# Kernel optimization log

Measured on AMD Instinct MI355X. Metric: run time of the kernel, lower is better.

## Reference

```python
import jax, jax.numpy as jnp
import numpy as np

DECAY_CONSTANT = 1.0


def _build_decay_matrices(weight, decay_value, S, dtype):
    """Build the row-repeat and col-repeat upper-triangular decay matrices.

    Wr[i, j] = w0[i] * (clip(dv0,0.9,1) ** (j-i) / C)   for j >= i, else 0
    Wc[i, j] = w1[j] *  clip(dv1,0.9,1) ** ((j-i) / C)  for j >= i, else 0
    """
    i = jnp.arange(S)[:, None]
    j = jnp.arange(S)[None, :]
    mask = j >= i
    # Clamp exponent to 0 in the masked-out (lower-triangular) region so the
    # power never overflows; values there are discarded by the mask anyway.
    e = jnp.where(mask, (j - i).astype(dtype), jnp.asarray(0.0, dtype))
    dv0 = jnp.clip(decay_value[0, 0], 0.9, 1.0).astype(dtype)
    dv1 = jnp.clip(decay_value[1, 0], 0.9, 1.0).astype(dtype)
    w0 = weight[0].astype(dtype)
    w1 = weight[1].astype(dtype)
    Wr = jnp.where(mask, w0[:, None] * ((dv0 ** e) / DECAY_CONSTANT), jnp.asarray(0.0, dtype))
    Wc = jnp.where(mask, w1[None, :] * (dv1 ** (e / DECAY_CONSTANT)), jnp.asarray(0.0, dtype))
    return Wr, Wc


def setup_inputs() -> dict:
    key = jax.random.key(0)
    kx, kw = jax.random.split(key)
    B, E, S = 4, 2048, 2048
    x = jax.random.normal(kx, (B, E, S), dtype=jnp.float32)
    weight = jax.random.normal(kw, (2, S), dtype=jnp.float32)
    bias = jnp.zeros((S,), dtype=jnp.float32)
    decay_value = jnp.ones((2, 1), dtype=jnp.float32)
    return {"x": x, "weight": weight, "bias": bias, "decay_value": decay_value}


def reference(x, weight, bias, decay_value):
    B, E, S = x.shape
    Wr, Wc = _build_decay_matrices(weight, decay_value, S, x.dtype)
    # x @ Wr + x @ Wc == x @ (Wr + Wc); contract the S axis.
    out = jnp.einsum('bes,st->bet', x, Wr + Wc)  # [B, E, S]
    out = out + bias.astype(x.dtype)
    return out
```

## Files before the change

### kernel.cpp

```cpp
#include <hip/hip_runtime.h>


#define S_LEN 2048
#define THREADS 256

__global__ __launch_bounds__(THREADS, 8)
void crcl_kernel(const float* __restrict__ x,
                 const float* __restrict__ weight,
                 const float* __restrict__ bias,
                 const float* __restrict__ decay,
                 float* __restrict__ out)
{
    __shared__ float carry[2][4];

    const int t    = (int)threadIdx.x;
    const int lane = t & 63;
    const int w    = t >> 6;
    const long row = (long)blockIdx.x;

    const float4* x4  = (const float4*)(x + row * (long)S_LEN);
    const float4* w04 = (const float4*)weight;
    const float4* w14 = (const float4*)(weight + S_LEN);
    const float4* b4  = (const float4*)bias;

    const float4 xa = x4[2 * t],  xb = x4[2 * t + 1];
    const float4 wa = w04[2 * t], wb = w04[2 * t + 1];
    const float4 va = w14[2 * t], vb = w14[2 * t + 1];
    const float4 ba = b4[2 * t],  bb = b4[2 * t + 1];

    const float dv0 = fminf(fmaxf(decay[0], 0.9f), 1.0f);
    const float dv1 = fminf(fmaxf(decay[1], 0.9f), 1.0f);

    const float xs[8] = {xa.x, xa.y, xa.z, xa.w, xb.x, xb.y, xb.z, xb.w};
    const float ws[8] = {wa.x, wa.y, wa.z, wa.w, wb.x, wb.y, wb.z, wb.w};

    float pc = 0.0f, qc = 0.0f;
#pragma unroll
    for (int k = 0; k < 8; ++k) {
        pc = fmaf(dv0, pc, xs[k] * ws[k]);
        qc = fmaf(dv1, qc, xs[k]);
    }

    float A8_0 = dv0 * dv0; A8_0 *= A8_0; A8_0 *= A8_0;
    float A8_1 = dv1 * dv1; A8_1 *= A8_1; A8_1 *= A8_1;

    float cp = pc, cq = qc;
    float k0 = A8_0, k1 = A8_1;
#pragma unroll
    for (int d = 1; d < 64; d <<= 1) {
        const float up = __shfl_up(cp, (unsigned)d, 64);
        const float uq = __shfl_up(cq, (unsigned)d, 64);
        if (lane >= d) {
            cp = fmaf(k0, up, cp);
            cq = fmaf(k1, uq, cq);
        }
        k0 *= k0;
        k1 *= k1;
    }
    float cin_p = __shfl_up(cp, 1u, 64);
    float cin_q = __shfl_up(cq, 1u, 64);
    if (lane == 0) { cin_p = 0.0f; cin_q = 0.0f; }

    if (lane == 63) { carry[0][w] = cp; carry[1][w] = cq; }
    __syncthreads();

    float A512_0 = A8_0, A512_1 = A8_1;
#pragma unroll
    for (int b = 0; b < 6; ++b) { A512_0 *= A512_0; A512_1 *= A512_1; }

    float cwp = 0.0f, cwq = 0.0f;
#pragma unroll
    for (int v = 0; v < 3; ++v) {
        if (v < w) {
            cwp = fmaf(cwp, A512_0, carry[0][v]);
            cwq = fmaf(cwq, A512_1, carry[1][v]);
        }
    }
    const float e8 = (float)(8 * lane);
    const float pwl_0 = exp2f(e8 * log2f(dv0));
    const float pwl_1 = exp2f(e8 * log2f(dv1));
    cin_p = fmaf(cwp, pwl_0, cin_p);
    cin_q = fmaf(cwq, pwl_1, cin_q);

    const float vs[8] = {va.x, va.y, va.z, va.w, vb.x, vb.y, vb.z, vb.w};
    const float bs[8] = {ba.x, ba.y, ba.z, ba.w, bb.x, bb.y, bb.z, bb.w};

    float p2 = cin_p, q2 = cin_q;
    float ys[8];
#pragma unroll
    for (int k = 0; k < 8; ++k) {
        p2 = fmaf(dv0, p2, xs[k] * ws[k]);
        q2 = fmaf(dv1, q2, xs[k]);
        ys[k] = fmaf(vs[k], q2, p2) + bs[k];
    }

    float4* o4 = (float4*)(out + row * (long)S_LEN);
    o4[2 * t]     = make_float4(ys[0], ys[1], ys[2], ys[3]);
    o4[2 * t + 1] = make_float4(ys[4], ys[5], ys[6], ys[7]);
}

extern "C" void kernel_launch(void* const* d_in, const int* in_sizes, int n_in,
                              void* d_out, int out_size, void* d_ws, size_t ws_size,
                              hipStream_t stream) {
    const float* x      = (const float*)d_in[0];
    const float* weight = (const float*)d_in[1];
    const float* bias   = (const float*)d_in[2];
    const float* decay  = (const float*)d_in[3];
    float* out = (float*)d_out;

    const int nrows = in_sizes[0] / S_LEN;
    hipLaunchKernelGGL(crcl_kernel, dim3(nrows), dim3(THREADS), 0, stream,
                       x, weight, bias, decay, out);
}
```

Measured before the change: 27.13 us.

## Split each row into two coalesced halves with interleaved scans

Each thread now loads float4s at index t and 256+t instead of two adjacent float4s, so every global load and store instruction touches a fully contiguous span across the wavefront. To keep the recurrence correct, two independent 4-element chunks are scanned per thread in parallel. The block-level carry combine is extended to eight wave segments. This doubles the wave-level shuffle scans in exchange for better-coalesced memory access and more independent work per step.

```diff
diff --git a/kernel.cpp b/kernel.cpp
--- a/kernel.cpp
+++ b/kernel.cpp
@@ -3,6 +3,8 @@
 
 #define S_LEN 2048
 #define THREADS 256
+
+typedef float f4 __attribute__((ext_vector_type(4)));
 
 __global__ __launch_bounds__(THREADS, 8)
 void crcl_kernel(const float* __restrict__ x,
@@ -11,92 +13,119 @@
                  const float* __restrict__ decay,
                  float* __restrict__ out)
 {
-    __shared__ float carry[2][4];
+    __shared__ float ctot[2][8];
 
     const int t    = (int)threadIdx.x;
     const int lane = t & 63;
     const int w    = t >> 6;
     const long row = (long)blockIdx.x;
 
-    const float4* x4  = (const float4*)(x + row * (long)S_LEN);
-    const float4* w04 = (const float4*)weight;
-    const float4* w14 = (const float4*)(weight + S_LEN);
-    const float4* b4  = (const float4*)bias;
+    const f4* x4  = (const f4*)(x + row * (long)S_LEN);
+    const f4* w04 = (const f4*)weight;
+    const f4* w14 = (const f4*)(weight + S_LEN);
+    const f4* b4  = (const f4*)bias;
 
-    const float4 xa = x4[2 * t],  xb = x4[2 * t + 1];
-    const float4 wa = w04[2 * t], wb = w04[2 * t + 1];
-    const float4 va = w14[2 * t], vb = w14[2 * t + 1];
-    const float4 ba = b4[2 * t],  bb = b4[2 * t + 1];
+    const int sA = t, sB = 256 + t;
+    const f4 xA = x4[sA],  xB = x4[sB];
+    const f4 wA = w04[sA], wB = w04[sB];
+    const f4 vA = w14[sA], vB = w14[sB];
+    const f4 bA = b4[sA],  bB = b4[sB];
 
     const float dv0 = fminf(fmaxf(decay[0], 0.9f), 1.0f);
     const float dv1 = fminf(fmaxf(decay[1], 0.9f), 1.0f);
 
-    const float xs[8] = {xa.x, xa.y, xa.z, xa.w, xb.x, xb.y, xb.z, xb.w};
-    const float ws[8] = {wa.x, wa.y, wa.z, wa.w, wb.x, wb.y, wb.z, wb.w};
+    float A4_0 = dv0 * dv0; A4_0 *= A4_0;
+    float A4_1 = dv1 * dv1; A4_1 *= A4_1;
+    float A256_0 = A4_0, A256_1 = A4_1;
+#pragma unroll
+    for (int b = 0; b < 6; ++b) { A256_0 *= A256_0; A256_1 *= A256_1; }
+    const float e4 = (float)(4 * lane);
+    const float pw0l = exp2f(e4 * log2f(dv0));
+    const float pw1l = exp2f(e4 * log2f(dv1));
 
-    float pc = 0.0f, qc = 0.0f;
+    float TAp = 0.0f, TAq = 0.0f, TBp = 0.0f, TBq = 0.0f;
 #pragma unroll
-    for (int k = 0; k < 8; ++k) {
-        pc = fmaf(dv0, pc, xs[k] * ws[k]);
-        qc = fmaf(dv1, qc, xs[k]);
+    for (int j = 0; j < 4; ++j) {
+        TAp = fmaf(dv0, TAp, xA[j] * wA[j]);
+        TAq = fmaf(dv1, TAq, xA[j]);
+        TBp = fmaf(dv0, TBp, xB[j] * wB[j]);
+        TBq = fmaf(dv1, TBq, xB[j]);
     }
 
-    float A8_0 = dv0 * dv0; A8_0 *= A8_0; A8_0 *= A8_0;
-    float A8_1 = dv1 * dv1; A8_1 *= A8_1; A8_1 *= A8_1;
-
-    float cp = pc, cq = qc;
-    float k0 = A8_0, k1 = A8_1;
+    float sAp = TAp, sAq = TAq, sBp = TBp, sBq = TBq;
+    float k0 = A4_0, k1 = A4_1;
 #pragma unroll
     for (int d = 1; d < 64; d <<= 1) {
-        const float up = __shfl_up(cp, (unsigned)d, 64);
-        const float uq = __shfl_up(cq, (unsigned)d, 64);
+        const float uAp = __shfl_up(sAp, (unsigned)d, 64);
+        const float uAq = __shfl_up(sAq, (unsigned)d, 64);
+        const float uBp = __shfl_up(sBp, (unsigned)d, 64);
+        const float uBq = __shfl_up(sBq, (unsigned)d, 64);
         if (lane >= d) {
-            cp = fmaf(k0, up, cp);
-            cq = fmaf(k1, uq, cq);
+            sAp = fmaf(k0, uAp, sAp);
+            sAq = fmaf(k1, uAq, sAq);
+            sBp = fmaf(k0, uBp, sBp);
+            sBq = fmaf(k1, uBq, sBq);
         }
         k0 *= k0;
         k1 *= k1;
     }
-    float cin_p = __shfl_up(cp, 1u, 64);
-    float cin_q = __shfl_up(cq, 1u, 64);
-    if (lane == 0) { cin_p = 0.0f; cin_q = 0.0f; }
+    float eAp = __shfl_up(sAp, 1u, 64);
+    float eAq = __shfl_up(sAq, 1u, 64);
+    float eBp = __shfl_up(sBp, 1u, 64);
+    float eBq = __shfl_up(sBq, 1u, 64);
+    if (lane == 0) { eAp = eAq = eBp = eBq = 0.0f; }
 
-    if (lane == 63) { carry[0][w] = cp; carry[1][w] = cq; }
+    if (lane == 63) {
+        ctot[0][w]     = sAp;  ctot[1][w]     = sAq;
+        ctot[0][4 + w] = sBp;  ctot[1][4 + w] = sBq;
+    }
     __syncthreads();
 
-    float A512_0 = A8_0, A512_1 = A8_1;
+    float GAp = 0.0f, GAq = 0.0f;
 #pragma unroll
-    for (int b = 0; b < 6; ++b) { A512_0 *= A512_0; A512_1 *= A512_1; }
-
-    float cwp = 0.0f, cwq = 0.0f;
-#pragma unroll
-    for (int v = 0; v < 3; ++v) {
-        if (v < w) {
-            cwp = fmaf(cwp, A512_0, carry[0][v]);
-            cwq = fmaf(cwq, A512_1, carry[1][v]);
+    for (int d = 0; d < 3; ++d) {
+        if (d < w) {
+            GAp = fmaf(A256_0, GAp, ctot[0][d]);
+            GAq = fmaf(A256_1, GAq, ctot[1][d]);
         }
     }
-    const float e8 = (float)(8 * lane);
-    const float pwl_0 = exp2f(e8 * log2f(dv0));
-    const float pwl_1 = exp2f(e8 * log2f(dv1));
-    cin_p = fmaf(cwp, pwl_0, cin_p);
-    cin_q = fmaf(cwq, pwl_1, cin_q);
-
-    const float vs[8] = {va.x, va.y, va.z, va.w, vb.x, vb.y, vb.z, vb.w};
-    const float bs[8] = {ba.x, ba.y, ba.z, ba.w, bb.x, bb.y, bb.z, bb.w};
-
-    float p2 = cin_p, q2 = cin_q;
-    float ys[8];
+    float GBp = 0.0f, GBq = 0.0f;
 #pragma unroll
-    for (int k = 0; k < 8; ++k) {
-        p2 = fmaf(dv0, p2, xs[k] * ws[k]);
-        q2 = fmaf(dv1, q2, xs[k]);
-        ys[k] = fmaf(vs[k], q2, p2) + bs[k];
+    for (int d = 0; d < 7; ++d) {
+        if (d < 4 + w) {
+            GBp = fmaf(A256_0, GBp, ctot[0][d]);
+            GBq = fmaf(A256_1, GBq, ctot[1][d]);
+        }
     }
 
-    float4* o4 = (float4*)(out + row * (long)S_LEN);
-    o4[2 * t]     = make_float4(ys[0], ys[1], ys[2], ys[3]);
-    o4[2 * t + 1] = make_float4(ys[4], ys[5], ys[6], ys[7]);
+    const float cinAp = fmaf(GAp, pw0l, eAp);
+    const float cinAq = fmaf(GAq, pw1l, eAq);
+    const float cinBp = fmaf(GBp, pw0l, eBp);
+    const float cinBq = fmaf(GBq, pw1l, eBq);
+
+    f4 yA, yB;
+    {
+        float p = cinAp, q = cinAq;
+#pragma unroll
+        for (int j = 0; j < 4; ++j) {
+            p = fmaf(dv0, p, xA[j] * wA[j]);
+            q = fmaf(dv1, q, xA[j]);
+            yA[j] = fmaf(vA[j], q, p) + bA[j];
+        }
+    }
+    {
+        float p = cinBp, q = cinBq;
+#pragma unroll
+        for (int j = 0; j < 4; ++j) {
+            p = fmaf(dv0, p, xB[j] * wB[j]);
+            q = fmaf(dv1, q, xB[j]);
+            yB[j] = fmaf(vB[j], q, p) + bB[j];
+        }
+    }
+
+    f4* o4 = (f4*)(out + row * (long)S_LEN);
+    o4[sA] = yA;
+    o4[sB] = yB;
 }
 
 extern "C" void kernel_launch(void* const* d_in, const int* in_sizes, int n_in,
```

Result: faster. 26.22 us (-3.4%).
